# Optimization experiments

Hardware: AMD Instinct MI355X
Metric: run time of the kernel (lower is better)

Reference implementation:

```python
import jax, jax.numpy as jnp
import numpy as np

DIM = 1024
INTER = 1024
E = 8            # n_routed_experts
TOP_K = 2        # n_activated_experts
ROUTE_SCALE = 1.0
B, S = 2, 1024


def setup_inputs() -> dict:
    key = jax.random.key(0)
    ks = jax.random.split(key, 8)
    scale = 0.02
    x = jax.random.normal(ks[0], (B, S, DIM), dtype=jnp.float32)
    gate_w = jax.random.normal(ks[1], (DIM, E), dtype=jnp.float32) * scale
    w1 = jax.random.normal(ks[2], (E, DIM, INTER), dtype=jnp.float32) * scale
    w2 = jax.random.normal(ks[3], (E, INTER, DIM), dtype=jnp.float32) * scale
    w3 = jax.random.normal(ks[4], (E, DIM, INTER), dtype=jnp.float32) * scale
    sw1 = jax.random.normal(ks[5], (DIM, INTER), dtype=jnp.float32) * scale
    sw2 = jax.random.normal(ks[6], (INTER, DIM), dtype=jnp.float32) * scale
    sw3 = jax.random.normal(ks[7], (DIM, INTER), dtype=jnp.float32) * scale
    return {"x": x, "gate_w": gate_w, "w1": w1, "w2": w2, "w3": w3,
            "sw1": sw1, "sw2": sw2, "sw3": sw3}


def reference(x, gate_w, w1, w2, w3, sw1, sw2, sw3):
    b, s, d = x.shape
    xt = x.reshape(-1, d)                      # [T, D]
    T = xt.shape[0]

    # --- TokenChoiceTopKRouter (score_func='softmax') ---
    scores = jax.nn.softmax((xt @ gate_w).astype(jnp.float32), axis=-1)  # [T, E]
    top_scores, top_idx = jax.lax.top_k(scores, TOP_K)                   # [T, K]
    top_scores = top_scores * ROUTE_SCALE

    # Dense combine weights [T, E]: scatter top-k routing weights per token.
    cw = jnp.zeros((T, E), dtype=xt.dtype)
    cw = cw.at[jnp.arange(T)[:, None], top_idx].set(top_scores.astype(xt.dtype))

    # --- GroupedExperts: SwiGLU per routed expert ---
    h1 = jnp.einsum('td,edh->teh', xt, w1)     # [T, E, INTER]
    h3 = jnp.einsum('td,edh->teh', xt, w3)
    h = jax.nn.silu(h1) * h3
    expert_out = jnp.einsum('teh,ehd->ted', h, w2)   # [T, E, D]

    # Combine: weighted sum over activated experts (zero weight elsewhere).
    routed = jnp.einsum('ted,te->td', expert_out, cw)

    # --- Shared expert (runs on all tokens) ---
    shared = (jax.nn.silu(xt @ sw1) * (xt @ sw3)) @ sw2

    return (routed + shared).reshape(b, s, d)
```

## Files before the change

### kernel.cpp

```cpp
#include <hip/hip_runtime.h>
#include <hip/hip_bf16.h>
#include <cstdint>
#include <cstddef>

#define DIM   1024
#define INTER 1024
#define NT    2048

typedef __attribute__((ext_vector_type(4))) float  f32x4;
typedef __attribute__((ext_vector_type(8))) short  s16x8;
typedef __attribute__((ext_vector_type(8))) unsigned short u16x8;

#define WS_CNT    0u
#define WS_SLOT   256u
#define WS_ASSIGN 33024u
#define WS_WT     65792u
#define WS_WTS2   98560u
#define WS_XB     131584u
#define WS_H      4325888u
#define WS_W1T    16908800u
#define WS_W3T    33686016u
#define WS_W2T    50463232u
#define WS_SW1T   67240448u
#define WS_SW3T   69337600u
#define WS_SW2T   71434752u
#define WS_NEED   73531904u
#define WS_OBUF   WS_W1T

__device__ __forceinline__ unsigned short f2bf(float f) {
    unsigned int u = __float_as_uint(f);
    return (unsigned short)((u + 0x7fffu + ((u >> 16) & 1u)) >> 16);
}
__device__ __forceinline__ float bf2f(unsigned short v) {
    return __uint_as_float(((unsigned int)v) << 16);
}

__device__ __forceinline__ void cp16(const void* g, void* l) {
    __builtin_amdgcn_global_load_lds((const __attribute__((address_space(1))) void*)g,
                                     (__attribute__((address_space(3))) void*)l, 16, 0, 0);
}

__global__ __launch_bounds__(256) void kconv_t(
    const float* __restrict__ w1, const float* __restrict__ w2, const float* __restrict__ w3,
    const float* __restrict__ sw1, const float* __restrict__ sw2, const float* __restrict__ sw3,
    unsigned short* __restrict__ w1t, unsigned short* __restrict__ w3t, unsigned short* __restrict__ w2t,
    unsigned short* __restrict__ sw1t, unsigned short* __restrict__ sw3t, unsigned short* __restrict__ sw2t)
{
    int z = blockIdx.z;
    const float* src; unsigned short* dst;
    if (z < 8)        { src = w1  + (size_t)z      * DIM * INTER; dst = w1t  + (size_t)z      * DIM * INTER; }
    else if (z < 16)  { src = w3  + (size_t)(z-8)  * DIM * INTER; dst = w3t  + (size_t)(z-8)  * DIM * INTER; }
    else if (z < 24)  { src = w2  + (size_t)(z-16) * DIM * INTER; dst = w2t  + (size_t)(z-16) * DIM * INTER; }
    else if (z == 24) { src = sw1; dst = sw1t; }
    else if (z == 25) { src = sw3; dst = sw3t; }
    else              { src = sw2; dst = sw2t; }

    __shared__ float tile[64][65];
    int tid = threadIdx.x;
    int r0 = blockIdx.y * 64, c0 = blockIdx.x * 64;
    int lr = tid >> 2, lcg = (tid & 3) * 16;
    const f32x4* srow = (const f32x4*)(src + (size_t)(r0 + lr) * 1024 + c0 + lcg);
    #pragma unroll
    for (int q = 0; q < 4; ++q) {
        f32x4 v = srow[q];
        #pragma unroll
        for (int j = 0; j < 4; ++j) tile[lr][lcg + q*4 + j] = v[j];
    }
    __syncthreads();
    int dc = tid >> 2, dkg = (tid & 3) * 16;
    u16x8 o0, o1;
    #pragma unroll
    for (int j = 0; j < 8; ++j) o0[j] = f2bf(tile[dkg + j][dc]);
    #pragma unroll
    for (int j = 0; j < 8; ++j) o1[j] = f2bf(tile[dkg + 8 + j][dc]);
    u16x8* drow = (u16x8*)(dst + (size_t)(c0 + dc) * 1024 + r0 + dkg);
    drow[0] = o0; drow[1] = o1;
}

__global__ __launch_bounds__(256) void kgate(const float* __restrict__ x, const float* __restrict__ gw,
                                             int* __restrict__ assign, float2* __restrict__ wts2,
                                             unsigned short* __restrict__ xb)
{
    int wid = threadIdx.x >> 6, lane = threadIdx.x & 63;
    int t = blockIdx.x * 4 + wid;
    const float* xrow = x + (size_t)t * DIM;

    float xr[16];
    float acc[8] = {0.f,0.f,0.f,0.f,0.f,0.f,0.f,0.f};
    #pragma unroll
    for (int j = 0; j < 16; ++j) {
        float xv = xrow[j * 64 + lane];
        xr[j] = xv;
        const f32x4* g = (const f32x4*)(gw + (size_t)(j * 64 + lane) * 8);
        f32x4 g0 = g[0], g1 = g[1];
        acc[0] += xv * g0[0]; acc[1] += xv * g0[1]; acc[2] += xv * g0[2]; acc[3] += xv * g0[3];
        acc[4] += xv * g1[0]; acc[5] += xv * g1[1]; acc[6] += xv * g1[2]; acc[7] += xv * g1[3];
    }
    #pragma unroll
    for (int j = 0; j < 16; ++j) xb[(size_t)t * DIM + j * 64 + lane] = f2bf(xr[j]);

    #pragma unroll
    for (int e = 0; e < 8; ++e) {
        float v = acc[e];
        v += __shfl_xor(v, 1);  v += __shfl_xor(v, 2);  v += __shfl_xor(v, 4);
        v += __shfl_xor(v, 8);  v += __shfl_xor(v, 16); v += __shfl_xor(v, 32);
        acc[e] = v;
    }
    float mx = acc[0];
    #pragma unroll
    for (int e = 1; e < 8; ++e) mx = fmaxf(mx, acc[e]);
    float p[8]; float se = 0.f;
    #pragma unroll
    for (int e = 0; e < 8; ++e) { p[e] = expf(acc[e] - mx); se += p[e]; }
    float inv = 1.0f / se;
    int i0 = 0; float b0 = p[0];
    #pragma unroll
    for (int e = 1; e < 8; ++e) if (p[e] > b0) { b0 = p[e]; i0 = e; }
    int i1 = -1; float b1 = -1.f;
    #pragma unroll
    for (int e = 0; e < 8; ++e) if (e != i0 && p[e] > b1) { b1 = p[e]; i1 = e; }
    if (lane == 0) {
        assign[t] = i0 | (i1 << 8);
        wts2[t] = make_float2(b0 * inv, b1 * inv);
    }
}

__global__ __launch_bounds__(256) void kscatter(const int* __restrict__ assign,
                                                const float2* __restrict__ wts2,
                                                int* __restrict__ cnt,
                                                int* __restrict__ slots,
                                                float* __restrict__ wts)
{
    __shared__ int h[8], pos[8];
    int tid = threadIdx.x, lane = tid & 63;
    if (tid < 8) h[tid] = 0;
    __syncthreads();

    for (int base = 0; base < NT; base += 256) {
        int a = assign[base + tid];
        int e0 = a & 255, e1 = (a >> 8) & 255;
        #pragma unroll
        for (int e = 0; e < 8; ++e) {
            unsigned long long m0 = __ballot(e0 == e);
            unsigned long long m1 = __ballot(e1 == e);
            if (lane == 0) {
                int c = __popcll(m0) + __popcll(m1);
                if (c) atomicAdd(&h[e], c);
            }
        }
    }
    __syncthreads();
    if (tid == 0) {
        int run = 0;
        #pragma unroll
        for (int e = 0; e < 8; ++e) {
            cnt[8 + e] = run; pos[e] = run;
            cnt[e] = h[e]; run += h[e];
        }
        cnt[16] = run;
    }
    __syncthreads();

    for (int base = 0; base < NT; base += 256) {
        int t = base + tid;
        int a = assign[t];
        float2 w = wts2[t];
        int e0 = a & 255, e1 = (a >> 8) & 255;
        unsigned long long lt = (1ull << lane) - 1ull;
        #pragma unroll
        for (int e = 0; e < 8; ++e) {
            unsigned long long m0 = __ballot(e0 == e);
            unsigned long long m1 = __ballot(e1 == e);
            int c = __popcll(m0) + __popcll(m1);
            int b = 0;
            if (lane == 0 && c) b = atomicAdd(&pos[e], c);
            b = __shfl(b, 0);
            if (e0 == e) { int r = __popcll(m0 & lt);                 slots[b + r] = t * 2;     wts[b + r] = w.x; }
            if (e1 == e) { int r = __popcll(m0) + __popcll(m1 & lt);  slots[b + r] = t * 2 + 1; wts[b + r] = w.y; }
        }
    }
}

__global__ __launch_bounds__(256) void kgemm1(
    const unsigned short* __restrict__ xb,
    const unsigned short* __restrict__ w1t, const unsigned short* __restrict__ w3t,
    const unsigned short* __restrict__ sw1t, const unsigned short* __restrict__ sw3t,
    const int* __restrict__ cnt, const int* __restrict__ slots,
    unsigned short* __restrict__ hbuf)
{
    int e = blockIdx.z;
    int m0 = blockIdx.y * 128;
    int n0 = blockIdx.x * 64;
    int n_rows, lbase;
    if (e < 8) { n_rows = cnt[e]; lbase = cnt[8 + e]; } else { n_rows = NT; lbase = 0; }
    if (m0 >= n_rows) return;
    int rm = min(128, n_rows - m0);

    const unsigned short* b1p = (e < 8) ? (w1t + (size_t)e * DIM * INTER) : sw1t;
    const unsigned short* b3p = (e < 8) ? (w3t + (size_t)e * DIM * INTER) : sw3t;

    __shared__ __align__(16) short As[2][128 * 64];
    __shared__ __align__(16) short B1s[2][64 * 64];
    __shared__ __align__(16) short B3s[2][64 * 64];
    __shared__ int rowTok[128];
    __shared__ int rowSlot[128];

    int tid = threadIdx.x;
    if (tid < 128) {
        int r = m0 + min(tid, rm - 1);
        int slot, tok;
        if (e < 8) { slot = slots[lbase + r]; tok = slot >> 1; }
        else       { tok = r; slot = 4096 + r; }
        rowTok[tid] = tok;
        rowSlot[tid] = slot;
    }
    __syncthreads();

    int wid = tid >> 6, lane = tid & 63;
    int wr = wid >> 1, wc = wid & 1;
    int swz_st = (((lane & 7) ^ (lane >> 3)) - (lane & 7)) * 16;

    const char* pA[4];
    #pragma unroll
    for (int q = 0; q < 4; ++q) {
        int row = (q * 4 + wid) * 8 + (lane >> 3);
        pA[q] = (const char*)(xb + (size_t)rowTok[row] * DIM) + (lane & 7) * 16 + swz_st;
    }
    const char* pB1[2]; const char* pB3[2];
    #pragma unroll
    for (int q = 0; q < 2; ++q) {
        int nrow = (q * 4 + wid) * 8 + (lane >> 3);
        pB1[q] = (const char*)(b1p + (size_t)(n0 + nrow) * DIM) + (lane & 7) * 16 + swz_st;
        pB3[q] = (const char*)(b3p + (size_t)(n0 + nrow) * DIM) + (lane & 7) * 16 + swz_st;
    }

    int loA[2], loB[2];
    #pragma unroll
    for (int ks = 0; ks < 2; ++ks) {
        int ch = ((ks * 4) + (lane >> 4)) ^ (lane & 7);
        loA[ks] = (wr * 64 + (lane & 15)) * 128 + ch * 16;
        loB[ks] = (wc * 32 + (lane & 15)) * 128 + ch * 16;
    }

    f32x4 acc1[4][2], acc3[4][2];
    #pragma unroll
    for (int m = 0; m < 4; ++m)
        #pragma unroll
        for (int n = 0; n < 2; ++n) { acc1[m][n] = (f32x4){0.f,0.f,0.f,0.f}; acc3[m][n] = (f32x4){0.f,0.f,0.f,0.f}; }

    #pragma unroll
    for (int q = 0; q < 4; ++q) { cp16(pA[q], (char*)As + (q * 4 + wid) * 1024); pA[q] += 128; }
    #pragma unroll
    for (int q = 0; q < 2; ++q) {
        cp16(pB1[q], (char*)B1s + (q * 4 + wid) * 1024); pB1[q] += 128;
        cp16(pB3[q], (char*)B3s + (q * 4 + wid) * 1024); pB3[q] += 128;
    }

    for (int tt = 0; tt < 8; ++tt) {
        #pragma unroll
        for (int half = 0; half < 2; ++half) {
            if (half == 0 || tt < 7) {
                #pragma unroll
                for (int q = 0; q < 4; ++q) {
                    cp16(pA[q], (char*)As + (half ^ 1) * 16384 + (q * 4 + wid) * 1024);
                    pA[q] += 128;
                }
                #pragma unroll
                for (int q = 0; q < 2; ++q) {
                    cp16(pB1[q], (char*)B1s + (half ^ 1) * 8192 + (q * 4 + wid) * 1024);
                    pB1[q] += 128;
                    cp16(pB3[q], (char*)B3s + (half ^ 1) * 8192 + (q * 4 + wid) * 1024);
                    pB3[q] += 128;
                }
                asm volatile("s_waitcnt vmcnt(8)" ::: "memory");
            } else {
                asm volatile("s_waitcnt vmcnt(0)" ::: "memory");
            }
            __builtin_amdgcn_sched_barrier(0);
            __builtin_amdgcn_s_barrier();
            __builtin_amdgcn_sched_barrier(0);

            #pragma unroll
            for (int ks = 0; ks < 2; ++ks) {
                s16x8 a[4];
                #pragma unroll
                for (int m = 0; m < 4; ++m)
                    a[m] = *(const s16x8*)((const char*)As + half * 16384 + m * 2048 + loA[ks]);
                #pragma unroll
                for (int n = 0; n < 2; ++n) {
                    s16x8 b1 = *(const s16x8*)((const char*)B1s + half * 8192 + n * 2048 + loB[ks]);
                    s16x8 b3 = *(const s16x8*)((const char*)B3s + half * 8192 + n * 2048 + loB[ks]);
                    #pragma unroll
                    for (int m = 0; m < 4; ++m) {
                        acc1[m][n] = __builtin_amdgcn_mfma_f32_16x16x32_bf16(a[m], b1, acc1[m][n], 0, 0, 0);
                        acc3[m][n] = __builtin_amdgcn_mfma_f32_16x16x32_bf16(a[m], b3, acc3[m][n], 0, 0, 0);
                    }
                }
            }
            __builtin_amdgcn_sched_barrier(0);
            __builtin_amdgcn_s_barrier();
            __builtin_amdgcn_sched_barrier(0);
        }
    }

    #pragma unroll
    for (int m = 0; m < 4; ++m) {
        int rbase = wr * 64 + m * 16 + (lane >> 4) * 4;
        #pragma unroll
        for (int r = 0; r < 4; ++r) {
            int row = rbase + r;
            if (row < rm) {
                int hrow = rowSlot[row];
                #pragma unroll
                for (int n = 0; n < 2; ++n) {
                    float v1 = acc1[m][n][r], v3 = acc3[m][n][r];
                    float hv = (v1 / (1.0f + __expf(-v1))) * v3;
                    int col = n0 + wc * 32 + n * 16 + (lane & 15);
                    hbuf[(size_t)hrow * INTER + col] = f2bf(hv);
                }
            }
        }
    }
}

__global__ __launch_bounds__(256) void kgemm2(
    const unsigned short* __restrict__ hbuf,
    const unsigned short* __restrict__ w2t, const unsigned short* __restrict__ sw2t,
    const int* __restrict__ cnt, const int* __restrict__ slots,
    unsigned short* __restrict__ obuf)
{
    int e = blockIdx.z;
    int m0 = blockIdx.y * 128;
    int n0 = blockIdx.x * 64;
    int n_rows, lbase;
    if (e < 8) { n_rows = cnt[e]; lbase = cnt[8 + e]; } else { n_rows = NT; lbase = 0; }
    if (m0 >= n_rows) return;
    int rm = min(128, n_rows - m0);
    const unsigned short* bp = (e < 8) ? (w2t + (size_t)e * DIM * INTER) : sw2t;

    __shared__ __align__(16) short As[2][128 * 64];
    __shared__ __align__(16) short Bs[2][64 * 64];
    __shared__ int rowH[128];

    int tid = threadIdx.x;
    if (tid < 128) {
        int r = m0 + min(tid, rm - 1);
        rowH[tid] = (e < 8) ? slots[lbase + r] : (4096 + r);
    }
    __syncthreads();

    int wid = tid >> 6, lane = tid & 63;
    int wr = wid >> 1, wc = wid & 1;
    int swz_st = (((lane & 7) ^ (lane >> 3)) - (lane & 7)) * 16;

    const char* pA[4];
    #pragma unroll
    for (int q = 0; q < 4; ++q) {
        int row = (q * 4 + wid) * 8 + (lane >> 3);
        pA[q] = (const char*)(hbuf + (size_t)rowH[row] * INTER) + (lane & 7) * 16 + swz_st;
    }
    const char* pB[2];
    #pragma unroll
    for (int q = 0; q < 2; ++q) {
        int nrow = (q * 4 + wid) * 8 + (lane >> 3);
        pB[q] = (const char*)(bp + (size_t)(n0 + nrow) * INTER) + (lane & 7) * 16 + swz_st;
    }

    int loA[2], loB[2];
    #pragma unroll
    for (int ks = 0; ks < 2; ++ks) {
        int ch = ((ks * 4) + (lane >> 4)) ^ (lane & 7);
        loA[ks] = (wr * 64 + (lane & 15)) * 128 + ch * 16;
        loB[ks] = (wc * 32 + (lane & 15)) * 128 + ch * 16;
    }

    f32x4 acc[4][2];
    #pragma unroll
    for (int m = 0; m < 4; ++m)
        #pragma unroll
        for (int n = 0; n < 2; ++n) acc[m][n] = (f32x4){0.f,0.f,0.f,0.f};

    #pragma unroll
    for (int q = 0; q < 4; ++q) { cp16(pA[q], (char*)As + (q * 4 + wid) * 1024); pA[q] += 128; }
    #pragma unroll
    for (int q = 0; q < 2; ++q) { cp16(pB[q], (char*)Bs + (q * 4 + wid) * 1024); pB[q] += 128; }

    for (int tt = 0; tt < 8; ++tt) {
        #pragma unroll
        for (int half = 0; half < 2; ++half) {
            if (half == 0 || tt < 7) {
                #pragma unroll
                for (int q = 0; q < 4; ++q) {
                    cp16(pA[q], (char*)As + (half ^ 1) * 16384 + (q * 4 + wid) * 1024);
                    pA[q] += 128;
                }
                #pragma unroll
                for (int q = 0; q < 2; ++q) {
                    cp16(pB[q], (char*)Bs + (half ^ 1) * 8192 + (q * 4 + wid) * 1024);
                    pB[q] += 128;
                }
                asm volatile("s_waitcnt vmcnt(6)" ::: "memory");
            } else {
                asm volatile("s_waitcnt vmcnt(0)" ::: "memory");
            }
            __builtin_amdgcn_sched_barrier(0);
            __builtin_amdgcn_s_barrier();
            __builtin_amdgcn_sched_barrier(0);

            #pragma unroll
            for (int ks = 0; ks < 2; ++ks) {
                s16x8 a[4];
                #pragma unroll
                for (int m = 0; m < 4; ++m)
                    a[m] = *(const s16x8*)((const char*)As + half * 16384 + m * 2048 + loA[ks]);
                #pragma unroll
                for (int n = 0; n < 2; ++n) {
                    s16x8 b = *(const s16x8*)((const char*)Bs + half * 8192 + n * 2048 + loB[ks]);
                    #pragma unroll
                    for (int m = 0; m < 4; ++m)
                        acc[m][n] = __builtin_amdgcn_mfma_f32_16x16x32_bf16(a[m], b, acc[m][n], 0, 0, 0);
                }
            }
            __builtin_amdgcn_sched_barrier(0);
            __builtin_amdgcn_s_barrier();
            __builtin_amdgcn_sched_barrier(0);
        }
    }

    #pragma unroll
    for (int m = 0; m < 4; ++m) {
        int rbase = wr * 64 + m * 16 + (lane >> 4) * 4;
        #pragma unroll
        for (int r = 0; r < 4; ++r) {
            int row = rbase + r;
            if (row < rm) {
                int orow = rowH[row];
                #pragma unroll
                for (int n = 0; n < 2; ++n) {
                    int col = n0 + wc * 32 + n * 16 + (lane & 15);
                    obuf[(size_t)orow * DIM + col] = f2bf(acc[m][n][r]);
                }
            }
        }
    }
}

__global__ __launch_bounds__(256) void kcombine(const unsigned short* __restrict__ obuf,
                                                const float2* __restrict__ wts2,
                                                float* __restrict__ out)
{
    int gid = blockIdx.x * 256 + threadIdx.x;
    int t = gid >> 7;
    int d0 = (gid & 127) * 8;
    float2 w = wts2[t];
    u16x8 r0 = *(const u16x8*)&obuf[(size_t)(2 * t)     * DIM + d0];
    u16x8 r1 = *(const u16x8*)&obuf[(size_t)(2 * t + 1) * DIM + d0];
    u16x8 rs = *(const u16x8*)&obuf[(size_t)(4096 + t)  * DIM + d0];
    f32x4 o0, o1;
    #pragma unroll
    for (int j = 0; j < 4; ++j) o0[j] = w.x * bf2f(r0[j]) + w.y * bf2f(r1[j]) + bf2f(rs[j]);
    #pragma unroll
    for (int j = 0; j < 4; ++j) o1[j] = w.x * bf2f(r0[4+j]) + w.y * bf2f(r1[4+j]) + bf2f(rs[4+j]);
    f32x4* dst = (f32x4*)&out[(size_t)t * DIM + d0];
    dst[0] = o0; dst[1] = o1;
}

extern "C" void kernel_launch(void* const* d_in, const int* in_sizes, int n_in,
                              void* d_out, int out_size, void* d_ws, size_t ws_size,
                              hipStream_t stream) {
    const float* x      = (const float*)d_in[0];
    const float* gate_w = (const float*)d_in[1];
    const float* w1     = (const float*)d_in[2];
    const float* w2     = (const float*)d_in[3];
    const float* w3     = (const float*)d_in[4];
    const float* sw1    = (const float*)d_in[5];
    const float* sw2    = (const float*)d_in[6];
    const float* sw3    = (const float*)d_in[7];
    float* out = (float*)d_out;

    if (ws_size < (size_t)WS_NEED) return;

    char* ws = (char*)d_ws;
    int*            cnt      = (int*)(ws + WS_CNT);
    int*            slots    = (int*)(ws + WS_SLOT);
    int*            assign   = (int*)(ws + WS_ASSIGN);
    float*          wts      = (float*)(ws + WS_WT);
    float2*         wts2     = (float2*)(ws + WS_WTS2);
    unsigned short* xb       = (unsigned short*)(ws + WS_XB);
    unsigned short* hbuf     = (unsigned short*)(ws + WS_H);
    unsigned short* w1t      = (unsigned short*)(ws + WS_W1T);
    unsigned short* w3t      = (unsigned short*)(ws + WS_W3T);
    unsigned short* w2t      = (unsigned short*)(ws + WS_W2T);
    unsigned short* sw1t     = (unsigned short*)(ws + WS_SW1T);
    unsigned short* sw3t     = (unsigned short*)(ws + WS_SW3T);
    unsigned short* sw2t     = (unsigned short*)(ws + WS_SW2T);
    unsigned short* obuf     = (unsigned short*)(ws + WS_OBUF);

    kconv_t<<<dim3(16, 16, 27), 256, 0, stream>>>(w1, w2, w3, sw1, sw2, sw3,
                                                  w1t, w3t, w2t, sw1t, sw3t, sw2t);
    kgate<<<dim3(NT / 4), 256, 0, stream>>>(x, gate_w, assign, wts2, xb);
    kscatter<<<dim3(1), 256, 0, stream>>>(assign, wts2, cnt, slots, wts);
    kgemm1<<<dim3(16, 16, 9), 256, 0, stream>>>(xb, w1t, w3t, sw1t, sw3t, cnt, slots, hbuf);
    kgemm2<<<dim3(16, 16, 9), 256, 0, stream>>>(hbuf, w2t, sw2t, cnt, slots, obuf);
    kcombine<<<dim3(NT * DIM / 8 / 256), 256, 0, stream>>>(obuf, wts2, out);
}
```

Before: 138.1 us.

## Fuse weight conversion into gate and gemm1 kernels to overlap work

Merges the w1/w3/shared transpose-convert blocks into the gate kernel launch and moves w2/sw2 conversion into the gemm1 launch as extra grid slices, so conversion of w2 overlaps with the first GEMM. Conversion tiles now cover 64x128 per block using a two-half shared tile. This removes a kernel launch and lets idle CUs during gemm1 do conversion work. The cost is larger static shared memory in the gemm1 kernel (66.5KB), which may lower occupancy, and block-scheduling interference between the two kinds of work.

```diff
diff --git a/kernel.cpp b/kernel.cpp
--- a/kernel.cpp
+++ b/kernel.cpp
@@ -40,49 +40,60 @@
                                      (__attribute__((address_space(3))) void*)l, 16, 0, 0);
 }
 
-__global__ __launch_bounds__(256) void kconv_t(
-    const float* __restrict__ w1, const float* __restrict__ w2, const float* __restrict__ w3,
-    const float* __restrict__ sw1, const float* __restrict__ sw2, const float* __restrict__ sw3,
-    unsigned short* __restrict__ w1t, unsigned short* __restrict__ w3t, unsigned short* __restrict__ w2t,
-    unsigned short* __restrict__ sw1t, unsigned short* __restrict__ sw3t, unsigned short* __restrict__ sw2t)
+__device__ __forceinline__ void conv_tile(const float* __restrict__ src,
+                                          unsigned short* __restrict__ dst,
+                                          int r0, int c0, char* smem)
 {
-    int z = blockIdx.z;
-    const float* src; unsigned short* dst;
-    if (z < 8)        { src = w1  + (size_t)z      * DIM * INTER; dst = w1t  + (size_t)z      * DIM * INTER; }
-    else if (z < 16)  { src = w3  + (size_t)(z-8)  * DIM * INTER; dst = w3t  + (size_t)(z-8)  * DIM * INTER; }
-    else if (z < 24)  { src = w2  + (size_t)(z-16) * DIM * INTER; dst = w2t  + (size_t)(z-16) * DIM * INTER; }
-    else if (z == 24) { src = sw1; dst = sw1t; }
-    else if (z == 25) { src = sw3; dst = sw3t; }
-    else              { src = sw2; dst = sw2t; }
-
-    __shared__ float tile[64][65];
+    float (*tile)[64][65] = (float (*)[64][65])smem;
     int tid = threadIdx.x;
-    int r0 = blockIdx.y * 64, c0 = blockIdx.x * 64;
     int lr = tid >> 2, lcg = (tid & 3) * 16;
-    const f32x4* srow = (const f32x4*)(src + (size_t)(r0 + lr) * 1024 + c0 + lcg);
-    #pragma unroll
-    for (int q = 0; q < 4; ++q) {
-        f32x4 v = srow[q];
-        #pragma unroll
-        for (int j = 0; j < 4; ++j) tile[lr][lcg + q*4 + j] = v[j];
+    #pragma unroll
+    for (int h = 0; h < 2; ++h) {
+        const f32x4* srow = (const f32x4*)(src + (size_t)(r0 + lr) * 1024 + c0 + h * 64 + lcg);
+        #pragma unroll
+        for (int q = 0; q < 4; ++q) {
+            f32x4 v = srow[q];
+            #pragma unroll
+            for (int j = 0; j < 4; ++j) tile[h][lr][lcg + q * 4 + j] = v[j];
+        }
     }
     __syncthreads();
     int dc = tid >> 2, dkg = (tid & 3) * 16;
-    u16x8 o0, o1;
-    #pragma unroll
-    for (int j = 0; j < 8; ++j) o0[j] = f2bf(tile[dkg + j][dc]);
-    #pragma unroll
-    for (int j = 0; j < 8; ++j) o1[j] = f2bf(tile[dkg + 8 + j][dc]);
-    u16x8* drow = (u16x8*)(dst + (size_t)(c0 + dc) * 1024 + r0 + dkg);
-    drow[0] = o0; drow[1] = o1;
-}
-
-__global__ __launch_bounds__(256) void kgate(const float* __restrict__ x, const float* __restrict__ gw,
-                                             int* __restrict__ assign, float2* __restrict__ wts2,
-                                             unsigned short* __restrict__ xb)
+    #pragma unroll
+    for (int h = 0; h < 2; ++h) {
+        u16x8 o0, o1;
+        #pragma unroll
+        for (int j = 0; j < 8; ++j) o0[j] = f2bf(tile[h][dkg + j][dc]);
+        #pragma unroll
+        for (int j = 0; j < 8; ++j) o1[j] = f2bf(tile[h][dkg + 8 + j][dc]);
+        u16x8* drow = (u16x8*)(dst + (size_t)(c0 + h * 64 + dc) * 1024 + r0 + dkg);
+        drow[0] = o0; drow[1] = o1;
+    }
+}
+
+__global__ __launch_bounds__(256) void kfat1(
+    const float* __restrict__ x, const float* __restrict__ gw,
+    const float* __restrict__ w1, const float* __restrict__ w3,
+    const float* __restrict__ sw1, const float* __restrict__ sw3,
+    unsigned short* __restrict__ w1t, unsigned short* __restrict__ w3t,
+    unsigned short* __restrict__ sw1t, unsigned short* __restrict__ sw3t,
+    int* __restrict__ assign, float2* __restrict__ wts2, unsigned short* __restrict__ xb)
 {
+    __shared__ __align__(16) char smem[33280];
+    int bid = blockIdx.x;
+    if (bid < 2304) {
+        int slab = bid >> 7, t = bid & 127;
+        int r0 = (t >> 3) * 64, c0 = (t & 7) * 128;
+        const float* src; unsigned short* dst;
+        if (slab < 8)        { src = w1 + (size_t)slab * DIM * INTER;       dst = w1t + (size_t)slab * DIM * INTER; }
+        else if (slab < 16)  { src = w3 + (size_t)(slab - 8) * DIM * INTER; dst = w3t + (size_t)(slab - 8) * DIM * INTER; }
+        else if (slab == 16) { src = sw1; dst = sw1t; }
+        else                 { src = sw3; dst = sw3t; }
+        conv_tile(src, dst, r0, c0, smem);
+        return;
+    }
     int wid = threadIdx.x >> 6, lane = threadIdx.x & 63;
-    int t = blockIdx.x * 4 + wid;
+    int t = (bid - 2304) * 4 + wid;
     const float* xrow = x + (size_t)t * DIM;
 
     float xr[16];
@@ -181,14 +192,28 @@
     }
 }
 
-__global__ __launch_bounds__(256) void kgemm1(
+__global__ __launch_bounds__(256) void kfat2(
     const unsigned short* __restrict__ xb,
     const unsigned short* __restrict__ w1t, const unsigned short* __restrict__ w3t,
     const unsigned short* __restrict__ sw1t, const unsigned short* __restrict__ sw3t,
     const int* __restrict__ cnt, const int* __restrict__ slots,
-    unsigned short* __restrict__ hbuf)
+    unsigned short* __restrict__ hbuf,
+    const float* __restrict__ w2, const float* __restrict__ sw2,
+    unsigned short* __restrict__ w2t, unsigned short* __restrict__ sw2t)
 {
-    int e = blockIdx.z;
+    __shared__ __align__(16) char smem[66560];
+    int z = blockIdx.z;
+    if (z >= 9) {
+        if (blockIdx.x >= 8) return;
+        int slab = z - 9;
+        const float* src; unsigned short* dst;
+        if (slab < 8) { src = w2 + (size_t)slab * DIM * INTER; dst = w2t + (size_t)slab * DIM * INTER; }
+        else          { src = sw2; dst = sw2t; }
+        conv_tile(src, dst, blockIdx.y * 64, blockIdx.x * 128, smem);
+        return;
+    }
+
+    int e = z;
     int m0 = blockIdx.y * 128;
     int n0 = blockIdx.x * 64;
     int n_rows, lbase;
@@ -199,11 +224,11 @@
     const unsigned short* b1p = (e < 8) ? (w1t + (size_t)e * DIM * INTER) : sw1t;
     const unsigned short* b3p = (e < 8) ? (w3t + (size_t)e * DIM * INTER) : sw3t;
 
-    __shared__ __align__(16) short As[2][128 * 64];
-    __shared__ __align__(16) short B1s[2][64 * 64];
-    __shared__ __align__(16) short B3s[2][64 * 64];
-    __shared__ int rowTok[128];
-    __shared__ int rowSlot[128];
+    char* sA  = smem;
+    char* sB1 = smem + 32768;
+    char* sB3 = smem + 49152;
+    int* rowTok  = (int*)(smem + 65536);
+    int* rowSlot = (int*)(smem + 66048);
 
     int tid = threadIdx.x;
     if (tid < 128) {
@@ -249,11 +274,11 @@
         for (int n = 0; n < 2; ++n) { acc1[m][n] = (f32x4){0.f,0.f,0.f,0.f}; acc3[m][n] = (f32x4){0.f,0.f,0.f,0.f}; }
 
     #pragma unroll
-    for (int q = 0; q < 4; ++q) { cp16(pA[q], (char*)As + (q * 4 + wid) * 1024); pA[q] += 128; }
+    for (int q = 0; q < 4; ++q) { cp16(pA[q], sA + (q * 4 + wid) * 1024); pA[q] += 128; }
     #pragma unroll
     for (int q = 0; q < 2; ++q) {
-        cp16(pB1[q], (char*)B1s + (q * 4 + wid) * 1024); pB1[q] += 128;
-        cp16(pB3[q], (char*)B3s + (q * 4 + wid) * 1024); pB3[q] += 128;
+        cp16(pB1[q], sB1 + (q * 4 + wid) * 1024); pB1[q] += 128;
+        cp16(pB3[q], sB3 + (q * 4 + wid) * 1024); pB3[q] += 128;
     }
 
     for (int tt = 0; tt < 8; ++tt) {
@@ -262,14 +287,14 @@
             if (half == 0 || tt < 7) {
                 #pragma unroll
                 for (int q = 0; q < 4; ++q) {
-                    cp16(pA[q], (char*)As + (half ^ 1) * 16384 + (q * 4 + wid) * 1024);
+                    cp16(pA[q], sA + (half ^ 1) * 16384 + (q * 4 + wid) * 1024);
                     pA[q] += 128;
                 }
                 #pragma unroll
                 for (int q = 0; q < 2; ++q) {
-                    cp16(pB1[q], (char*)B1s + (half ^ 1) * 8192 + (q * 4 + wid) * 1024);
+                    cp16(pB1[q], sB1 + (half ^ 1) * 8192 + (q * 4 + wid) * 1024);
                     pB1[q] += 128;
-                    cp16(pB3[q], (char*)B3s + (half ^ 1) * 8192 + (q * 4 + wid) * 1024);
+                    cp16(pB3[q], sB3 + (half ^ 1) * 8192 + (q * 4 + wid) * 1024);
                     pB3[q] += 128;
                 }
                 asm volatile("s_waitcnt vmcnt(8)" ::: "memory");
@@ -285,11 +310,11 @@
                 s16x8 a[4];
                 #pragma unroll
                 for (int m = 0; m < 4; ++m)
-                    a[m] = *(const s16x8*)((const char*)As + half * 16384 + m * 2048 + loA[ks]);
+                    a[m] = *(const s16x8*)(sA + half * 16384 + m * 2048 + loA[ks]);
                 #pragma unroll
                 for (int n = 0; n < 2; ++n) {
-                    s16x8 b1 = *(const s16x8*)((const char*)B1s + half * 8192 + n * 2048 + loB[ks]);
-                    s16x8 b3 = *(const s16x8*)((const char*)B3s + half * 8192 + n * 2048 + loB[ks]);
+                    s16x8 b1 = *(const s16x8*)(sB1 + half * 8192 + n * 2048 + loB[ks]);
+                    s16x8 b3 = *(const s16x8*)(sB3 + half * 8192 + n * 2048 + loB[ks]);
                     #pragma unroll
                     for (int m = 0; m < 4; ++m) {
                         acc1[m][n] = __builtin_amdgcn_mfma_f32_16x16x32_bf16(a[m], b1, acc1[m][n], 0, 0, 0);
@@ -496,11 +521,11 @@
     unsigned short* sw2t     = (unsigned short*)(ws + WS_SW2T);
     unsigned short* obuf     = (unsigned short*)(ws + WS_OBUF);
 
-    kconv_t<<<dim3(16, 16, 27), 256, 0, stream>>>(w1, w2, w3, sw1, sw2, sw3,
-                                                  w1t, w3t, w2t, sw1t, sw3t, sw2t);
-    kgate<<<dim3(NT / 4), 256, 0, stream>>>(x, gate_w, assign, wts2, xb);
+    kfat1<<<dim3(2816), 256, 0, stream>>>(x, gate_w, w1, w3, sw1, sw3,
+                                          w1t, w3t, sw1t, sw3t, assign, wts2, xb);
     kscatter<<<dim3(1), 256, 0, stream>>>(assign, wts2, cnt, slots, wts);
-    kgemm1<<<dim3(16, 16, 9), 256, 0, stream>>>(xb, w1t, w3t, sw1t, sw3t, cnt, slots, hbuf);
+    kfat2<<<dim3(16, 16, 18), 256, 0, stream>>>(xb, w1t, w3t, sw1t, sw3t, cnt, slots, hbuf,
+                                                w2, sw2, w2t, sw2t);
     kgemm2<<<dim3(16, 16, 9), 256, 0, stream>>>(hbuf, w2t, sw2t, cnt, slots, obuf);
-    kcombine<<<dim3(NT * DIM / 8 / 256), 256, 0, stream>>>(obuf, wts2, out);
-}
+    kcombine<<<dim3(1024), 256, 0, stream>>>(obuf, wts2, out);
+}
```

Result: faster. 128.9 us (-6.7%).
